# Optimization experiments

Measured on AMD Instinct MI355X. Metric: run time of the kernel, lower is better.

The kernel has to match this reference:

```python
import jax, jax.numpy as jnp
import numpy as np
from jax import lax

N_FRAMES = 256

def _conv(x, w, b):
    # NCHW conv, stride 3 on mel axis (matches MOSNet CNN that collapses mels 81->27->9->3->1)
    y = lax.conv_general_dilated(x, w, window_strides=(1, 3),
                                 padding=((1, 1), (1, 1)),
                                 dimension_numbers=('NCHW', 'OIHW', 'NCHW'))
    return jax.nn.relu(y + b[None, :, None, None])

def _lstm(x, Wih, Whh, bih, bhh, reverse=False):
    # x: [T, B, D] -> hs: [T, B, H]; PyTorch gate order i, f, g, o
    Bsz, H = x.shape[1], Whh.shape[1]
    bias = bih + bhh
    def step(carry, xt):
        h, c = carry
        z = xt @ Wih.T + h @ Whh.T + bias
        i, f, g, o = jnp.split(z, 4, axis=-1)
        c = jax.nn.sigmoid(f) * c + jax.nn.sigmoid(i) * jnp.tanh(g)
        h = jax.nn.sigmoid(o) * jnp.tanh(c)
        return (h, c), h
    init = (jnp.zeros((Bsz, H), x.dtype), jnp.zeros((Bsz, H), x.dtype))
    _, hs = lax.scan(step, init, x, reverse=reverse)
    return hs

def setup_inputs():
    key = jax.random.key(0)
    ks = jax.random.split(key, 24)
    B, T, M = 16, 4096, 81
    chans = [1, 16, 32, 64, 128]
    H = 128
    FC_IN = 2 * H * N_FRAMES  # 65536
    FC_H = 128
    s = 0.05
    inp = {'audio': jax.random.normal(ks[0], (B, T, M), jnp.float32),
           'sample_lengths': jnp.full((B,), T, dtype=jnp.int32)}
    for li in range(4):
        inp['w%d' % li] = jax.random.normal(ks[1 + 2 * li], (chans[li + 1], chans[li], 3, 3), jnp.float32) * s
        inp['b%d' % li] = jnp.zeros((chans[li + 1],), jnp.float32)
    D = chans[-1]
    for d, off in (('f', 9), ('b', 13)):
        inp['Wih_' + d] = jax.random.normal(ks[off], (4 * H, D), jnp.float32) * s
        inp['Whh_' + d] = jax.random.normal(ks[off + 1], (4 * H, H), jnp.float32) * s
        inp['bih_' + d] = jnp.zeros((4 * H,), jnp.float32)
        inp['bhh_' + d] = jnp.zeros((4 * H,), jnp.float32)
    inp['fc1_w'] = jax.random.normal(ks[17], (FC_H, FC_IN), jnp.float32) * 0.005
    inp['fc1_b'] = jnp.zeros((FC_H,), jnp.float32)
    inp['fs_w'] = jax.random.normal(ks[18], (1, FC_H), jnp.float32) * s
    inp['fs_b'] = jnp.zeros((1,), jnp.float32)
    return inp

def reference(audio, w0, b0, w1, b1, w2, b2, w3, b3,
              Wih_f, Whh_f, bih_f, bhh_f, Wih_b, Whh_b, bih_b, bhh_b,
              fc1_w, fc1_b, fs_w, fs_b, sample_lengths):
    B, T, M = audio.shape
    F = T // N_FRAMES  # all lengths == T, multiple of N_FRAMES -> all frames full
    x = audio.reshape(B * F, 1, N_FRAMES, M)   # [BF, 1, nf, mels]
    for w, b in ((w0, b0), (w1, b1), (w2, b2), (w3, b3)):
        x = _conv(x, w, b)                      # mel axis 81->27->9->3->1
    x = x[..., 0].transpose(2, 0, 1)            # [nf, BF, C]
    h_f = _lstm(x, Wih_f, Whh_f, bih_f, bhh_f)
    h_b = _lstm(x, Wih_b, Whh_b, bih_b, bhh_b, reverse=True)
    h = jnp.concatenate([h_f, h_b], axis=-1).transpose(1, 0, 2)  # [BF, nf, 2H]
    flat = h.reshape(B * F, -1)                 # time-major flatten, matches view(1,-1)
    z = jax.nn.relu(flat @ fc1_w.T + fc1_b)     # dropout is identity at inference
    score = jax.nn.sigmoid(z @ fs_w.T + fs_b) * 4.0 + 1.0  # mos range [1,5]
    frames = score.reshape(B, F)
    utt = frames.mean(axis=1)
    return utt, frames
```

## Files before the change

kernel.cpp:

```cpp
#include <hip/hip_runtime.h>
#include <hip/hip_fp16.h>

#define BF 256
#define TSTEPS 256

typedef _Float16 h8_t __attribute__((ext_vector_type(8)));
typedef _Float16 h4_t __attribute__((ext_vector_type(4)));
typedef float f4_t __attribute__((ext_vector_type(4)));

union H8 { uint4 u; h8_t v; };
union H4 { uint2 u; h4_t v; };
union U2H4 { uint2 u; __half h[4]; };

static __device__ __forceinline__ float sigmoidf_(float x) {
    return 1.f / (1.f + __expf(-x));
}
static __device__ __forceinline__ float tanhf_(float x) {
    return 1.f - 2.f / (__expf(2.f * x) + 1.f);
}

static __device__ __forceinline__ void wg_barrier_lds() {
    __builtin_amdgcn_sched_barrier(0);
    asm volatile("s_waitcnt lgkmcnt(0)" ::: "memory");
    __builtin_amdgcn_s_barrier();
    __builtin_amdgcn_sched_barrier(0);
}

static __device__ __forceinline__ void pack_one(const float* __restrict__ src,
                                                __half* __restrict__ dst,
                                                int OC, int IC, int KS,
                                                int oc_str, int ic_str, int k_str, int i) {
    int grp = KS / 4;
    int j = i % grp;
    int oc = (i / grp) % OC;
    int g = (i / (grp * OC)) & 3;
    int chunk = i / (grp * OC * 4);
    int CPK = IC / KS;
    int cc = chunk % CPK;
    int khw = chunk / CPK;
    int ic = cc * KS + g * grp + j;
    dst[i] = __float2half(src[(long)oc * oc_str + (long)ic * ic_str + khw * k_str]);
}

__global__ __launch_bounds__(256) void prep_k(
        const float* __restrict__ w0, const float* __restrict__ w1,
        const float* __restrict__ w2, const float* __restrict__ w3,
        const float* __restrict__ Wihf, const float* __restrict__ Wihb,
        const float* __restrict__ Whhf, const float* __restrict__ Whhb,
        float* __restrict__ w0t, __half* __restrict__ w1p,
        __half* __restrict__ w2p, __half* __restrict__ w3p,
        __half* __restrict__ wfp, __half* __restrict__ wbp,
        __half* __restrict__ whhfp, __half* __restrict__ whhbp) {
    int i = blockIdx.x * 256 + threadIdx.x;
    if (i < 144) { int oc = i / 9, rem = i % 9; w0t[rem * 16 + oc] = w0[i]; return; }
    i -= 144;
    if (i < 4608) { pack_one(w1, w1p, 32, 16, 16, 144, 9, 1, i); return; }
    i -= 4608;
    if (i < 18432) { pack_one(w2, w2p, 64, 32, 32, 288, 9, 1, i); return; }
    i -= 18432;
    if (i < 73728) { pack_one(w3, w3p, 128, 64, 32, 576, 9, 1, i); return; }
    i -= 73728;
    if (i < 65536) { pack_one(Wihf, wfp, 512, 128, 32, 128, 1, 0, i); return; }
    i -= 65536;
    if (i < 65536) { pack_one(Wihb, wbp, 512, 128, 32, 128, 1, 0, i); return; }
    i -= 65536;
    if (i < 65536) { pack_one(Whhf, whhfp, 512, 128, 32, 128, 1, 0, i); return; }
    i -= 65536;
    if (i < 65536) { pack_one(Whhb, whhbp, 512, 128, 32, 128, 1, 0, i); return; }
}

__global__ void pack_wf16(const float* __restrict__ src, __half* __restrict__ dst,
                          int OC, int IC, int KS,
                          int oc_str, int ic_str, int k_str, int total) {
    int i = blockIdx.x * 256 + threadIdx.x;
    if (i >= total) return;
    pack_one(src, dst, OC, IC, KS, oc_str, ic_str, k_str, i);
}

__global__ __launch_bounds__(256) void conv0_k(const float* __restrict__ in,
                                               const float* __restrict__ wT,
                                               const float* __restrict__ bias,
                                               __half* __restrict__ out) {
    __shared__ float wsm[9][16];
    __shared__ float bs[16];
    int tid = threadIdx.x;
    if (tid < 144) wsm[tid / 16][tid % 16] = wT[tid];
    if (tid < 16) bs[tid] = bias[tid];
    __syncthreads();
    int gid = blockIdx.x * 256 + tid;
    int ow = gid % 27;
    int t = (gid / 27) % 256;
    int bf = gid / (27 * 256);
    float acc[16];
#pragma unroll
    for (int o = 0; o < 16; o++) acc[o] = bs[o];
    int iw0 = ow * 3 - 1;
#pragma unroll
    for (int kh = 0; kh < 3; kh++) {
        int tt = t + kh - 1;
        if ((unsigned)tt >= 256u) continue;
        const float* ip = in + ((long)bf * 256 + tt) * 81;
#pragma unroll
        for (int kw = 0; kw < 3; kw++) {
            int iw = iw0 + kw;
            if ((unsigned)iw >= 81u) continue;
            float x = ip[iw];
#pragma unroll
            for (int o = 0; o < 16; o++) acc[o] += x * wsm[kh * 3 + kw][o];
        }
    }
    __half2* op = (__half2*)(out + (long)gid * 16);
#pragma unroll
    for (int o = 0; o < 8; o++)
        op[o] = __floats2half2_rn(fmaxf(acc[2 * o], 0.f), fmaxf(acc[2 * o + 1], 0.f));
}

template<int IC, int OC, int WIN, int WOUT, int KS>
__global__ __launch_bounds__(256) void convM_k(const __half* __restrict__ in,
                                               const __half* __restrict__ wp,
                                               const float* __restrict__ bias,
                                               __half* __restrict__ out) {
    constexpr int NT = OC / 16;
    constexpr int CPK = IC / KS;
    constexpr int NCHUNK = 9 * CPK;
    constexpr int GRP = KS / 4;
    int tid = threadIdx.x;
    int lane = tid & 63;
    int wv = tid >> 6;
    int l15 = lane & 15;
    int g = lane >> 4;
    int m = blockIdx.x * 64 + wv * 16 + l15;
    int ow = m % WOUT;
    int t = (m / WOUT) % 256;
    int bf = m / (WOUT * 256);

    f4_t acc[NT];
#pragma unroll
    for (int nt = 0; nt < NT; nt++)
#pragma unroll
        for (int r = 0; r < 4; r++) acc[nt][r] = 0.f;

#pragma unroll
    for (int chunk = 0; chunk < NCHUNK; chunk++) {
        int khw = chunk / CPK, cc = chunk % CPK;
        int kh = khw / 3;
        int kw = khw - kh * 3;
        int tt = t + kh - 1;
        int iw = ow * 3 + kw - 1;
        bool ok = ((unsigned)tt < 256u) && ((unsigned)iw < (unsigned)WIN);
        long aoff = ok ? (((long)(bf * 256 + tt) * WIN + iw) * IC + cc * KS + g * GRP) : 0;
        if constexpr (KS == 32) {
            H8 af;
            af.u = *(const uint4*)(in + aoff);
            if (!ok) af.u = make_uint4(0u, 0u, 0u, 0u);
#pragma unroll
            for (int nt = 0; nt < NT; nt++) {
                H8 bf8;
                bf8.u = *(const uint4*)(wp + ((long)(chunk * 4 + g) * OC + nt * 16 + l15) * GRP);
                acc[nt] = __builtin_amdgcn_mfma_f32_16x16x32_f16(af.v, bf8.v, acc[nt], 0, 0, 0);
            }
        } else {
            H4 af;
            af.u = *(const uint2*)(in + aoff);
            if (!ok) af.u = make_uint2(0u, 0u);
#pragma unroll
            for (int nt = 0; nt < NT; nt++) {
                H4 bf4;
                bf4.u = *(const uint2*)(wp + ((long)(chunk * 4 + g) * OC + nt * 16 + l15) * GRP);
                acc[nt] = __builtin_amdgcn_mfma_f32_16x16x16f16(af.v, bf4.v, acc[nt], 0, 0, 0);
            }
        }
    }
    int orow = blockIdx.x * 64 + wv * 16 + g * 4;
#pragma unroll
    for (int nt = 0; nt < NT; nt++) {
        int oc = nt * 16 + l15;
        float b = bias[oc];
#pragma unroll
        for (int r = 0; r < 4; r++) {
            float v = fmaxf(acc[nt][r] + b, 0.f);
            out[(long)(orow + r) * OC + oc] = __float2half(v);
        }
    }
}

__global__ __launch_bounds__(256) void gates_k(const __half* __restrict__ X,
                                               const __half* __restrict__ wpf,
                                               const __half* __restrict__ wpb,
                                               const float* __restrict__ bf1,
                                               const float* __restrict__ bf2,
                                               const float* __restrict__ bb1,
                                               const float* __restrict__ bb2,
                                               __half* __restrict__ Gf,
                                               __half* __restrict__ Gb) {
    int dir = blockIdx.z;
    const __half* wp = dir ? wpb : wpf;
    const float* b1 = dir ? bb1 : bf1;
    const float* b2 = dir ? bb2 : bf2;
    __half* G = dir ? Gb : Gf;
    int tid = threadIdx.x;
    int lane = tid & 63;
    int wv = tid >> 6;
    int l15 = lane & 15;
    int g = lane >> 4;
    long r0 = (long)blockIdx.x * 128 + wv * 32;
    int n0 = blockIdx.y * 128;

    f4_t acc[2][8];
#pragma unroll
    for (int s = 0; s < 2; s++)
#pragma unroll
        for (int nt = 0; nt < 8; nt++)
#pragma unroll
            for (int r = 0; r < 4; r++) acc[s][nt][r] = 0.f;

#pragma unroll
    for (int chunk = 0; chunk < 4; chunk++) {
        H8 a0, a1;
        a0.u = *(const uint4*)(X + (r0 + l15) * 128 + chunk * 32 + g * 8);
        a1.u = *(const uint4*)(X + (r0 + 16 + l15) * 128 + chunk * 32 + g * 8);
#pragma unroll
        for (int nt = 0; nt < 8; nt++) {
            H8 bw;
            bw.u = *(const uint4*)(wp + ((long)(chunk * 4 + g) * 512 + n0 + nt * 16 + l15) * 8);
            acc[0][nt] = __builtin_amdgcn_mfma_f32_16x16x32_f16(a0.v, bw.v, acc[0][nt], 0, 0, 0);
            acc[1][nt] = __builtin_amdgcn_mfma_f32_16x16x32_f16(a1.v, bw.v, acc[1][nt], 0, 0, 0);
        }
    }
    int b = (int)(r0 >> 8);
#pragma unroll
    for (int nt = 0; nt < 8; nt++) {
        int col = n0 + nt * 16 + l15;
        float bias = b1[col] + b2[col];
        long base = ((long)b * 512 + col) * 256;
#pragma unroll
        for (int s = 0; s < 2; s++) {
            int tb = (int)(r0 & 255) + s * 16 + g * 4;
            U2H4 pk;
            if (!dir) {
#pragma unroll
                for (int r = 0; r < 4; r++) pk.h[r] = __float2half(acc[s][nt][r] + bias);
                *(uint2*)(G + base + tb) = pk.u;
            } else {
#pragma unroll
                for (int r = 0; r < 4; r++) pk.h[3 - r] = __float2half(acc[s][nt][r] + bias);
                *(uint2*)(G + base + (252 - tb)) = pk.u;
            }
        }
    }
}

__global__ __launch_bounds__(512, 2) void lstm_k(const __half* __restrict__ Gf,
                                                 const __half* __restrict__ Gb,
                                                 const __half* __restrict__ whhfp,
                                                 const __half* __restrict__ whhbp,
                                                 __half* __restrict__ flat) {
    int bid = blockIdx.x;
    int dir = bid >> 7;
    int b0 = (bid & 127) * 2;
    const __half* G = dir ? Gb : Gf;
    const __half* wp = dir ? whhbp : whhfp;
    int tid = threadIdx.x;
    int w = tid >> 6;
    int lane = tid & 63;
    int l15 = lane & 15;
    int g2 = lane >> 4;
    int chn = l15 >> 3;
    int r = l15 & 3;
    int bit2 = (l15 >> 2) & 1;
    int ua = w * 16 + g2 * 4 + r;
    bool wrt = bit2 && ((r & 1) == 0);

    H8 afr[4][4];
#pragma unroll
    for (int k = 0; k < 4; k++) {
        int gate = k * 128 + w * 16 + l15;
#pragma unroll
        for (int c = 0; c < 4; c++)
            afr[k][c].u = *(const uint4*)(wp + ((long)((c * 4 + g2) * 512 + gate)) * 8);
    }

    __shared__ __align__(16) __half hbuf[2][2][128];
    if (tid < 256) hbuf[0][tid >> 7][tid & 127] = __float2half(0.f);
    __syncthreads();

    const __half* gb0 = G + (((long)(b0 + chn) * 512) + bit2 * 256 + ua) * 256;
    const __half* gb1 = gb0 + 128 * 256;

    float cst = 0.f;
    float ma = bit2 ? 2.f : 1.f;
    float mb = bit2 ? 2.f : 1.f;
    float cb = bit2 ? -1.f : 0.f;
    const f4_t zero4 = {0.f, 0.f, 0.f, 0.f};

    H8 gc0, gc1, gn0, gn1;
    gc0.u = *(const uint4*)(gb0);
    gc1.u = *(const uint4*)(gb1);
    long fbase = (long)(b0 + chn) * 65536 + dir * 128 + ua;

    for (int to = 0; to < 32; to++) {
        if (to < 31) {
            gn0.u = *(const uint4*)(gb0 + (to + 1) * 8);
            gn1.u = *(const uint4*)(gb1 + (to + 1) * 8);
        }
#pragma unroll
        for (int ti = 0; ti < 8; ti++) {
            int s = to * 8 + ti;
            int p = s & 1;
            H8 bfr[4];
#pragma unroll
            for (int c = 0; c < 4; c++)
                bfr[c].u = *(const uint4*)(&hbuf[p][chn][c * 32 + g2 * 8]);

            f4_t acc[4];
#pragma unroll
            for (int k = 0; k < 4; k++)
                acc[k] = __builtin_amdgcn_mfma_f32_16x16x32_f16(afr[k][0].v, bfr[0].v,
                                                                zero4, 0, 0, 0);
#pragma unroll
            for (int c = 1; c < 4; c++)
#pragma unroll
                for (int k = 0; k < 4; k++)
                    acc[k] = __builtin_amdgcn_mfma_f32_16x16x32_f16(afr[k][c].v, bfr[c].v,
                                                                    acc[k], 0, 0, 0);
            f4_t aA, aB;
#pragma unroll
            for (int e = 0; e < 4; e++) {
                aA[e] = bit2 ? acc[2][e] : acc[0][e];
                aB[e] = bit2 ? acc[3][e] : acc[1][e];
            }
            float loA = (r & 1) ? aA[1] : aA[0];
            float hiA = (r & 1) ? aA[3] : aA[2];
            float eA = (r & 2) ? hiA : loA;
            float loB = (r & 1) ? aB[1] : aB[0];
            float hiB = (r & 1) ? aB[3] : aB[2];
            float eB = (r & 2) ? hiB : loB;

            float za = eA + (float)gc0.v[ti];
            float zb = eB + (float)gc1.v[ti];
            float sa = sigmoidf_(ma * za);
            float fa = sa * mb + cb;
            float sb = sigmoidf_(zb);
            float grecv = __shfl_xor(fa, 4, 64);
            float cn = sb * cst + fa * grecv;
            cst = cn;
            float tc = tanhf_(cn);
            float tcr = __shfl_xor(tc, 4, 64);
            float h = sb * tcr;
            float hp = __shfl_xor(h, 1, 64);
            if (wrt) {
                __half2 h2 = __floats2half2_rn(h, hp);
                int ts = dir ? (255 - s) : s;
                *(__half2*)(&hbuf[p ^ 1][chn][ua]) = h2;
                *(__half2*)(flat + fbase + (long)ts * 256) = h2;
            }
            wg_barrier_lds();
        }
        gc0 = gn0;
        gc1 = gn1;
    }
}

__global__ __launch_bounds__(256) void fc1m_k(const __half* __restrict__ flat,
                                              const __half* __restrict__ wp,
                                              float* __restrict__ z) {
    int tid = threadIdx.x;
    int lane = tid & 63;
    int wv = tid >> 6;
    int l15 = lane & 15;
    int g = lane >> 4;
    int m0 = blockIdx.x * 64 + wv * 16;
    long k0 = (long)blockIdx.y * 1024;

    f4_t acc[8];
#pragma unroll
    for (int nt = 0; nt < 8; nt++)
#pragma unroll
        for (int r = 0; r < 4; r++) acc[nt][r] = 0.f;

    for (int c = 0; c < 32; c++) {
        long chunk = (k0 >> 5) + c;
        H8 af;
        af.u = *(const uint4*)(flat + (long)(m0 + l15) * 65536 + k0 + c * 32 + g * 8);
#pragma unroll
        for (int nt = 0; nt < 8; nt++) {
            H8 bw;
            bw.u = *(const uint4*)(wp + ((chunk * 4 + g) * 128 + nt * 16 + l15) * 8);
            acc[nt] = __builtin_amdgcn_mfma_f32_16x16x32_f16(af.v, bw.v, acc[nt], 0, 0, 0);
        }
    }
#pragma unroll
    for (int nt = 0; nt < 8; nt++)
#pragma unroll
        for (int r = 0; r < 4; r++)
            atomicAdd(&z[(m0 + g * 4 + r) * 128 + nt * 16 + l15], acc[nt][r]);
}

__global__ void zero_k(float* __restrict__ p, int n) {
    int i = blockIdx.x * 256 + threadIdx.x;
    if (i < n) p[i] = 0.f;
}

__global__ __launch_bounds__(256) void head_k(const float* __restrict__ z,
                                              const float* __restrict__ b1,
                                              const float* __restrict__ fsw,
                                              const float* __restrict__ fsb,
                                              float* __restrict__ out) {
    __shared__ float sf[256];
    int r = threadIdx.x;
    float acc = fsb[0];
#pragma unroll
    for (int j4 = 0; j4 < 32; j4++) {
        float4 zv = *(const float4*)&z[r * 128 + j4 * 4];
        float4 bv = *(const float4*)&b1[j4 * 4];
        float4 wv = *(const float4*)&fsw[j4 * 4];
        acc += fmaxf(zv.x + bv.x, 0.f) * wv.x;
        acc += fmaxf(zv.y + bv.y, 0.f) * wv.y;
        acc += fmaxf(zv.z + bv.z, 0.f) * wv.z;
        acc += fmaxf(zv.w + bv.w, 0.f) * wv.w;
    }
    float val = sigmoidf_(acc) * 4.f + 1.f;
    out[16 + r] = val;
    sf[r] = val;
    __syncthreads();
    if (r < 16) {
        float m = 0.f;
#pragma unroll
        for (int f = 0; f < 16; f++) m += sf[r * 16 + f];
        out[r] = m * (1.f / 16.f);
    }
}

extern "C" void kernel_launch(void* const* d_in, const int* in_sizes, int n_in,
                              void* d_out, int out_size, void* d_ws, size_t ws_size,
                              hipStream_t stream) {
    const float* audio = (const float*)d_in[0];
    const float* w0 = (const float*)d_in[2];
    const float* b0 = (const float*)d_in[3];
    const float* w1 = (const float*)d_in[4];
    const float* b1 = (const float*)d_in[5];
    const float* w2 = (const float*)d_in[6];
    const float* b2 = (const float*)d_in[7];
    const float* w3 = (const float*)d_in[8];
    const float* b3 = (const float*)d_in[9];
    const float* Wih_f = (const float*)d_in[10];
    const float* Whh_f = (const float*)d_in[11];
    const float* bih_f = (const float*)d_in[12];
    const float* bhh_f = (const float*)d_in[13];
    const float* Wih_b = (const float*)d_in[14];
    const float* Whh_b = (const float*)d_in[15];
    const float* bih_b = (const float*)d_in[16];
    const float* bhh_b = (const float*)d_in[17];
    const float* fc1_w = (const float*)d_in[18];
    const float* fc1_b = (const float*)d_in[19];
    const float* fs_w = (const float*)d_in[20];
    const float* fs_b = (const float*)d_in[21];
    float* out = (float*)d_out;

    char* ws = (char*)d_ws;
    __half* Gf    = (__half*)(ws);
    __half* out1  = (__half*)(ws);
    __half* fc1p  = (__half*)(ws);
    __half* Gb    = (__half*)(ws + 67108864);
    __half* flat16= (__half*)(ws + 134217728);
    __half* out0  = (__half*)(ws + 134217728);
    __half* X     = (__half*)(ws + 201326592);
    __half* out2  = (__half*)(ws + 218103808);
    char* rd = ws + 243269632;
    float*  w0t   = (float*)(rd);
    __half* w1p   = (__half*)(rd + 1024);
    __half* w2p   = (__half*)(rd + 10240);
    __half* w3p   = (__half*)(rd + 47104);
    __half* wfp   = (__half*)(rd + 194560);
    __half* wbp   = (__half*)(rd + 325632);
    __half* whhfp = (__half*)(rd + 456704);
    __half* whhbp = (__half*)(rd + 587776);
    float*  zbuf  = (float*)(rd + 718848);

    prep_k<<<1403, 256, 0, stream>>>(w0, w1, w2, w3, Wih_f, Wih_b, Whh_f, Whh_b,
                                     w0t, w1p, w2p, w3p, wfp, wbp, whhfp, whhbp);

    conv0_k<<<6912, 256, 0, stream>>>(audio, w0t, b0, out0);
    convM_k<16, 32, 27, 9, 16><<<9216, 256, 0, stream>>>(out0, w1p, b1, out1);
    convM_k<32, 64, 9, 3, 32><<<3072, 256, 0, stream>>>(out1, w2p, b2, out2);
    convM_k<64, 128, 3, 1, 32><<<1024, 256, 0, stream>>>(out2, w3p, b3, X);

    gates_k<<<dim3(512, 4, 2), 256, 0, stream>>>(X, wfp, wbp, bih_f, bhh_f,
                                                 bih_b, bhh_b, Gf, Gb);

    lstm_k<<<256, 512, 0, stream>>>(Gf, Gb, whhfp, whhbp, flat16);

    pack_wf16<<<32768, 256, 0, stream>>>(fc1_w, fc1p, 128, 65536, 32, 65536, 1, 0, 8388608);
    zero_k<<<128, 256, 0, stream>>>(zbuf, 256 * 128);
    fc1m_k<<<dim3(4, 64), 256, 0, stream>>>(flat16, fc1p, zbuf);
    head_k<<<1, 256, 0, stream>>>(zbuf, fc1_b, fs_w, fs_b, out);
}
```

Before: 537.5 us.

## Spread LSTM recurrence over 16 waves with repacked Whh and one gate per lane

The recurrent LSTM kernel now launches 1024 threads per block instead of 512. The Whh weights are repacked so each wave computes two 16-row MFMA tiles instead of four. Each lane owns one gate value, and the cell update combines gates through lane shuffles, so per-step serial MFMA work and register pressure fall at the cost of more waves per barrier and scalar half stores. Sigmoid and tanh also switch to the hardware reciprocal intrinsic instead of a division.

Measured after the change: 532.1 us. About the same (-1.0%).

```diff
diff --git a/kernel.cpp b/kernel.cpp
--- a/kernel.cpp
+++ b/kernel.cpp
@@ -13,10 +13,10 @@
 union U2H4 { uint2 u; __half h[4]; };
 
 static __device__ __forceinline__ float sigmoidf_(float x) {
-    return 1.f / (1.f + __expf(-x));
+    return __builtin_amdgcn_rcpf(1.f + __expf(-x));
 }
 static __device__ __forceinline__ float tanhf_(float x) {
-    return 1.f - 2.f / (__expf(2.f * x) + 1.f);
+    return 1.f - 2.f * __builtin_amdgcn_rcpf(__expf(2.f * x) + 1.f);
 }
 
 static __device__ __forceinline__ void wg_barrier_lds() {
@@ -40,6 +40,19 @@
     int khw = chunk / CPK;
     int ic = cc * KS + g * grp + j;
     dst[i] = __float2half(src[(long)oc * oc_str + (long)ic * ic_str + khw * k_str]);
+}
+
+static __device__ __forceinline__ void pack_whh_one(const float* __restrict__ src,
+                                                    __half* __restrict__ dst, int i) {
+    int j = i & 7;
+    int prow = (i >> 3) & 511;
+    int cg = i >> 12;
+    int g = cg & 3, chunk = cg >> 2;
+    int t = prow >> 4, rr = prow & 15;
+    int cls = rr >> 2, du = rr & 3;
+    int orig = cls * 128 + t * 4 + du;
+    int ic = chunk * 32 + g * 8 + j;
+    dst[i] = __float2half(src[orig * 128 + ic]);
 }
 
 __global__ __launch_bounds__(256) void prep_k(
@@ -64,9 +77,9 @@
     i -= 65536;
     if (i < 65536) { pack_one(Wihb, wbp, 512, 128, 32, 128, 1, 0, i); return; }
     i -= 65536;
-    if (i < 65536) { pack_one(Whhf, whhfp, 512, 128, 32, 128, 1, 0, i); return; }
+    if (i < 65536) { pack_whh_one(Whhf, whhfp, i); return; }
     i -= 65536;
-    if (i < 65536) { pack_one(Whhb, whhbp, 512, 128, 32, 128, 1, 0, i); return; }
+    if (i < 65536) { pack_whh_one(Whhb, whhbp, i); return; }
 }
 
 __global__ void pack_wf16(const float* __restrict__ src, __half* __restrict__ dst,
@@ -250,11 +263,11 @@
     }
 }
 
-__global__ __launch_bounds__(512, 2) void lstm_k(const __half* __restrict__ Gf,
-                                                 const __half* __restrict__ Gb,
-                                                 const __half* __restrict__ whhfp,
-                                                 const __half* __restrict__ whhbp,
-                                                 __half* __restrict__ flat) {
+__global__ __launch_bounds__(1024, 4) void lstm_k(const __half* __restrict__ Gf,
+                                                  const __half* __restrict__ Gb,
+                                                  const __half* __restrict__ whhfp,
+                                                  const __half* __restrict__ whhbp,
+                                                  __half* __restrict__ flat) {
     int bid = blockIdx.x;
     int dir = bid >> 7;
     int b0 = (bid & 127) * 2;
@@ -266,43 +279,38 @@
     int l15 = lane & 15;
     int g2 = lane >> 4;
     int chn = l15 >> 3;
-    int r = l15 & 3;
-    int bit2 = (l15 >> 2) & 1;
-    int ua = w * 16 + g2 * 4 + r;
-    bool wrt = bit2 && ((r & 1) == 0);
-
-    H8 afr[4][4];
-#pragma unroll
-    for (int k = 0; k < 4; k++) {
-        int gate = k * 128 + w * 16 + l15;
+    int u8 = l15 & 7;
+    int unit = w * 8 + u8;
+    int tsel = (u8 >> 2) & 1;
+    int du = u8 & 3;
+
+    H8 afr[2][4];
+#pragma unroll
+    for (int t = 0; t < 2; t++) {
+        int prow = (w * 2 + t) * 16 + l15;
 #pragma unroll
         for (int c = 0; c < 4; c++)
-            afr[k][c].u = *(const uint4*)(wp + ((long)((c * 4 + g2) * 512 + gate)) * 8);
+            afr[t][c].u = *(const uint4*)(wp + ((long)((c * 4 + g2) * 512 + prow)) * 8);
     }
 
     __shared__ __align__(16) __half hbuf[2][2][128];
     if (tid < 256) hbuf[0][tid >> 7][tid & 127] = __float2half(0.f);
     __syncthreads();
 
-    const __half* gb0 = G + (((long)(b0 + chn) * 512) + bit2 * 256 + ua) * 256;
-    const __half* gb1 = gb0 + 128 * 256;
+    const __half* gb0 = G + (((long)(b0 + chn) * 512) + g2 * 128 + unit) * 256;
 
     float cst = 0.f;
-    float ma = bit2 ? 2.f : 1.f;
-    float mb = bit2 ? 2.f : 1.f;
-    float cb = bit2 ? -1.f : 0.f;
+    float ma = (g2 == 2) ? 2.f : 1.f;
+    float mb = ma;
+    float cb = (g2 == 2) ? -1.f : 0.f;
     const f4_t zero4 = {0.f, 0.f, 0.f, 0.f};
 
-    H8 gc0, gc1, gn0, gn1;
-    gc0.u = *(const uint4*)(gb0);
-    gc1.u = *(const uint4*)(gb1);
-    long fbase = (long)(b0 + chn) * 65536 + dir * 128 + ua;
+    H8 gc, gn;
+    gc.u = *(const uint4*)(gb0);
+    long fbase = (long)(b0 + chn) * 65536 + dir * 128 + unit;
 
     for (int to = 0; to < 32; to++) {
-        if (to < 31) {
-            gn0.u = *(const uint4*)(gb0 + (to + 1) * 8);
-            gn1.u = *(const uint4*)(gb1 + (to + 1) * 8);
-        }
+        if (to < 31) gn.u = *(const uint4*)(gb0 + (to + 1) * 8);
 #pragma unroll
         for (int ti = 0; ti < 8; ti++) {
             int s = to * 8 + ti;
@@ -312,52 +320,45 @@
             for (int c = 0; c < 4; c++)
                 bfr[c].u = *(const uint4*)(&hbuf[p][chn][c * 32 + g2 * 8]);
 
-            f4_t acc[4];
-#pragma unroll
-            for (int k = 0; k < 4; k++)
-                acc[k] = __builtin_amdgcn_mfma_f32_16x16x32_f16(afr[k][0].v, bfr[0].v,
+            f4_t acc[2];
+#pragma unroll
+            for (int t = 0; t < 2; t++)
+                acc[t] = __builtin_amdgcn_mfma_f32_16x16x32_f16(afr[t][0].v, bfr[0].v,
                                                                 zero4, 0, 0, 0);
 #pragma unroll
             for (int c = 1; c < 4; c++)
 #pragma unroll
-                for (int k = 0; k < 4; k++)
-                    acc[k] = __builtin_amdgcn_mfma_f32_16x16x32_f16(afr[k][c].v, bfr[c].v,
-                                                                    acc[k], 0, 0, 0);
-            f4_t aA, aB;
-#pragma unroll
-            for (int e = 0; e < 4; e++) {
-                aA[e] = bit2 ? acc[2][e] : acc[0][e];
-                aB[e] = bit2 ? acc[3][e] : acc[1][e];
-            }
-            float loA = (r & 1) ? aA[1] : aA[0];
-            float hiA = (r & 1) ? aA[3] : aA[2];
-            float eA = (r & 2) ? hiA : loA;
-            float loB = (r & 1) ? aB[1] : aB[0];
-            float hiB = (r & 1) ? aB[3] : aB[2];
-            float eB = (r & 2) ? hiB : loB;
-
-            float za = eA + (float)gc0.v[ti];
-            float zb = eB + (float)gc1.v[ti];
-            float sa = sigmoidf_(ma * za);
-            float fa = sa * mb + cb;
-            float sb = sigmoidf_(zb);
-            float grecv = __shfl_xor(fa, 4, 64);
-            float cn = sb * cst + fa * grecv;
+                for (int t = 0; t < 2; t++)
+                    acc[t] = __builtin_amdgcn_mfma_f32_16x16x32_f16(afr[t][c].v, bfr[c].v,
+                                                                    acc[t], 0, 0, 0);
+            f4_t at;
+#pragma unroll
+            for (int e = 0; e < 4; e++) at[e] = tsel ? acc[1][e] : acc[0][e];
+            float lo = (du & 1) ? at[1] : at[0];
+            float hi = (du & 1) ? at[3] : at[2];
+            float ev = (du & 2) ? hi : lo;
+
+            float z = ev + (float)gc.v[ti];
+            float a = sigmoidf_(ma * z) * mb + cb;
+
+            float x1 = __shfl_xor(a, 32, 64);
+            float pi = a * x1;
+            float x2 = __shfl_xor(pi, 16, 64);
+            float cn = a * cst + x2;
             cst = cn;
             float tc = tanhf_(cn);
-            float tcr = __shfl_xor(tc, 4, 64);
-            float h = sb * tcr;
-            float hp = __shfl_xor(h, 1, 64);
-            if (wrt) {
-                __half2 h2 = __floats2half2_rn(h, hp);
+            float x3 = __shfl_xor(tc, 32, 64);
+            float h = a * x3;
+
+            if (g2 == 3) {
+                __half hh = __float2half(h);
                 int ts = dir ? (255 - s) : s;
-                *(__half2*)(&hbuf[p ^ 1][chn][ua]) = h2;
-                *(__half2*)(flat + fbase + (long)ts * 256) = h2;
+                hbuf[p ^ 1][chn][unit] = hh;
+                flat[fbase + (long)ts * 256] = hh;
             }
             wg_barrier_lds();
         }
-        gc0 = gn0;
-        gc1 = gn1;
+        gc = gn;
     }
 }
 
@@ -488,7 +489,7 @@
     gates_k<<<dim3(512, 4, 2), 256, 0, stream>>>(X, wfp, wbp, bih_f, bhh_f,
                                                  bih_b, bhh_b, Gf, Gb);
 
-    lstm_k<<<256, 512, 0, stream>>>(Gf, Gb, whhfp, whhbp, flat16);
+    lstm_k<<<256, 1024, 0, stream>>>(Gf, Gb, whhfp, whhbp, flat16);
 
     pack_wf16<<<32768, 256, 0, stream>>>(fc1_w, fc1p, 128, 65536, 32, 65536, 1, 0, 8388608);
     zero_k<<<128, 256, 0, stream>>>(zbuf, 256 * 128);
```
